# Performance work log

Measured on AMD Instinct MI355X. Metric: run time of the kernel, lower is better.

The kernel has to match this reference:

```python
import jax, jax.numpy as jnp
import numpy as np

N = 100000      # nodes
E = 3200000     # edges (before self-loops)
IN = 1          # input feature dim
H1, C = 4, 8    # layer1: 4 heads x 8 channels; layer2: 1 head x 8 channels
NEG_SLOPE = 0.2


def setup_inputs() -> dict:
    key = jax.random.key(0)
    ks = jax.random.split(key, 10)
    x = jax.random.normal(ks[0], (N, IN), jnp.float32)
    edge_index = jax.random.randint(ks[1], (2, E), 0, N, dtype=jnp.int32)
    # layer 1 params (GATConv(1, 8, heads=4))
    W1 = jax.random.normal(ks[2], (IN, H1 * C), jnp.float32) * 0.5
    a_src1 = jax.random.normal(ks[3], (H1, C), jnp.float32) * 0.5
    a_dst1 = jax.random.normal(ks[4], (H1, C), jnp.float32) * 0.5
    b1 = jnp.zeros((H1 * C,), jnp.float32)
    # layer 2 params (GATConv(32, 8, heads=1))
    W2 = jax.random.normal(ks[5], (H1 * C, C), jnp.float32) * 0.2
    a_src2 = jax.random.normal(ks[6], (1, C), jnp.float32) * 0.5
    a_dst2 = jax.random.normal(ks[7], (1, C), jnp.float32) * 0.5
    b2 = jnp.zeros((C,), jnp.float32)
    return {"x": x, "edge_index": edge_index, "W1": W1, "a_src1": a_src1,
            "a_dst1": a_dst1, "b1": b1, "W2": W2, "a_src2": a_src2,
            "a_dst2": a_dst2, "b2": b2}


def _gat_layer(x, src, dst, W, a_s, a_d, b, heads, ch):
    # Linear transform per head: [N, heads, ch]
    h = (x @ W).reshape(-1, heads, ch)
    # per-node attention logits
    al_s = jnp.einsum('nhc,hc->nh', h, a_s)  # [N, H]
    al_d = jnp.einsum('nhc,hc->nh', h, a_d)  # [N, H]
    # per-edge logits (message src -> dst)
    e = jax.nn.leaky_relu(al_s[src] + al_d[dst], NEG_SLOPE)  # [E', H]
    # segment softmax over incoming edges of each dst node
    m = jax.ops.segment_max(e, dst, num_segments=N)          # [N, H]
    e = jnp.exp(e - m[dst])
    s = jax.ops.segment_sum(e, dst, num_segments=N)          # [N, H]
    alpha = e / s[dst]                                       # [E', H]
    # weighted scatter-add aggregation
    out = jax.ops.segment_sum(h[src] * alpha[:, :, None], dst, num_segments=N)
    return out.reshape(N, heads * ch) + b


def reference(x, edge_index, W1, a_src1, a_dst1, b1, W2, a_src2, a_dst2, b2):
    loops = jnp.arange(N, dtype=edge_index.dtype)
    src = jnp.concatenate([edge_index[0], loops])  # add self-loops (PyG default)
    dst = jnp.concatenate([edge_index[1], loops])
    h = _gat_layer(x, src, dst, W1, a_src1, a_dst1, b1, H1, C)
    h = jax.nn.relu(h)
    out = _gat_layer(h, src, dst, W2, a_src2, a_dst2, b2, 1, C)
    return out
```

## Files before the change

kernel.cpp:

```cpp
#include <hip/hip_runtime.h>
#include <hip/hip_bf16.h>

#define NEG_SLOPE 0.2f



__global__ void scatter_count(const int* __restrict__ ei, int* __restrict__ percnt,
                              int E) {
    __shared__ int cnt[2048];
    int t = threadIdx.x;
    int chunk = (E + gridDim.x - 1) / gridDim.x;
    int lo = blockIdx.x * chunk;
    int hi = min(E, lo + chunk);
    const int* dei = ei + E;
    for (int i = t; i < 2048; i += 1024) cnt[i] = 0;
    __syncthreads();
    bool vec = ((E & 3) == 0);
    int lo4 = (lo + 3) & ~3;
    int end4 = hi & ~3;
    if (vec && end4 > lo4) {
        for (int e = lo + t; e < lo4; e += 1024)
            atomicAdd(&cnt[dei[e] >> 6], 1);
        const int4* dei4 = (const int4*)dei;
        for (int v = (lo4 >> 2) + t; v < (end4 >> 2); v += 1024) {
            int4 d = dei4[v];
            atomicAdd(&cnt[d.x >> 6], 1);
            atomicAdd(&cnt[d.y >> 6], 1);
            atomicAdd(&cnt[d.z >> 6], 1);
            atomicAdd(&cnt[d.w >> 6], 1);
        }
        for (int e = end4 + t; e < hi; e += 1024)
            atomicAdd(&cnt[dei[e] >> 6], 1);
    } else {
        for (int e = lo + t; e < hi; e += 1024)
            atomicAdd(&cnt[dei[e] >> 6], 1);
    }
    __syncthreads();
    int* myp = percnt + blockIdx.x * 2048;
    for (int i = t; i < 2048; i += 1024) myp[i] = cnt[i];
}

__global__ void scan_bucket(int* __restrict__ percnt, int* __restrict__ gcnt,
                            int NBLK) {
    int wid = (blockIdx.x * blockDim.x + threadIdx.x) >> 6;
    int lane = threadIdx.x & 63;
    if (wid >= 2048) return;
    int base = lane * 4;
    int c0 = (base + 0 < NBLK) ? percnt[(size_t)(base + 0) * 2048 + wid] : 0;
    int c1 = (base + 1 < NBLK) ? percnt[(size_t)(base + 1) * 2048 + wid] : 0;
    int c2 = (base + 2 < NBLK) ? percnt[(size_t)(base + 2) * 2048 + wid] : 0;
    int c3 = (base + 3 < NBLK) ? percnt[(size_t)(base + 3) * 2048 + wid] : 0;
    int p1 = c0, p2 = c0 + c1, p3 = c0 + c1 + c2;
    int lsum = p3 + c3;
    int v = lsum;
    #pragma unroll
    for (int o = 1; o < 64; o <<= 1) {
        int u = __shfl_up(v, o, 64);
        if (lane >= o) v += u;
    }
    int excl = v - lsum;
    if (base + 0 < NBLK) percnt[(size_t)(base + 0) * 2048 + wid] = excl;
    if (base + 1 < NBLK) percnt[(size_t)(base + 1) * 2048 + wid] = excl + p1;
    if (base + 2 < NBLK) percnt[(size_t)(base + 2) * 2048 + wid] = excl + p2;
    if (base + 3 < NBLK) percnt[(size_t)(base + 3) * 2048 + wid] = excl + p3;
    if (lane == 63) gcnt[wid] = excl + lsum;
}

__global__ void scan_init(const int* __restrict__ gcnt,
                          int* __restrict__ gbase, int* __restrict__ gcursor,
                          const float* __restrict__ W1,
                          const float* __restrict__ as1,
                          const float* __restrict__ ad1,
                          float* __restrict__ consts) {
    __shared__ int buf[512];
    int t = threadIdx.x;
    if (t < 8) {
        int h = t & 3;
        const float* a = (t < 4) ? as1 : ad1;
        float s = 0.f;
        #pragma unroll
        for (int c = 0; c < 8; ++c)
            s += W1[h * 8 + c] * a[h * 8 + c];
        consts[t] = s;
    }
    int c0 = gcnt[t * 4], c1 = gcnt[t * 4 + 1], c2 = gcnt[t * 4 + 2], c3 = gcnt[t * 4 + 3];
    int sum = c0 + c1 + c2 + c3;
    buf[t] = sum;
    __syncthreads();
    for (int o = 1; o < 512; o <<= 1) {
        int add = (t >= o) ? buf[t - o] : 0;
        __syncthreads();
        buf[t] += add;
        __syncthreads();
    }
    int base = buf[t] - sum;
    gbase[t * 4] = base;     gcursor[t * 4] = base;     base += c0;
    gbase[t * 4 + 1] = base; gcursor[t * 4 + 1] = base; base += c1;
    gbase[t * 4 + 2] = base; gcursor[t * 4 + 2] = base; base += c2;
    gbase[t * 4 + 3] = base; gcursor[t * 4 + 3] = base;
}

__global__ void scatter_write(const int* __restrict__ ei,
                              const int* __restrict__ gbase,
                              const int* __restrict__ percnt,
                              unsigned int* __restrict__ pairs, int E) {
    __shared__ int cnt[2048];
    __shared__ int basel[2048];
    int t = threadIdx.x;
    int chunk = (E + gridDim.x - 1) / gridDim.x;
    int lo = blockIdx.x * chunk;
    int hi = min(E, lo + chunk);
    const int* dei = ei + E;
    const int* myp = percnt + blockIdx.x * 2048;
    for (int i = t; i < 2048; i += 1024) {
        cnt[i] = 0;
        basel[i] = gbase[i] + myp[i];
    }
    __syncthreads();
    bool vec = ((E & 3) == 0);
    int lo4 = (lo + 3) & ~3;
    int end4 = hi & ~3;
    if (vec && end4 > lo4) {
        for (int e = lo + t; e < lo4; e += 1024) {
            int s = ei[e], d = dei[e];
            int bk = d >> 6;
            int loc = atomicAdd(&cnt[bk], 1);
            pairs[basel[bk] + loc] = (unsigned)s | ((unsigned)(d & 63) << 17);
        }
        const int4* sei4 = (const int4*)ei;
        const int4* dei4 = (const int4*)dei;
        for (int v = (lo4 >> 2) + t; v < (end4 >> 2); v += 1024) {
            int4 sv = sei4[v];
            int4 dv = dei4[v];
            int bk0 = dv.x >> 6, bk1 = dv.y >> 6, bk2 = dv.z >> 6, bk3 = dv.w >> 6;
            int l0 = atomicAdd(&cnt[bk0], 1);
            pairs[basel[bk0] + l0] = (unsigned)sv.x | ((unsigned)(dv.x & 63) << 17);
            int l1 = atomicAdd(&cnt[bk1], 1);
            pairs[basel[bk1] + l1] = (unsigned)sv.y | ((unsigned)(dv.y & 63) << 17);
            int l2 = atomicAdd(&cnt[bk2], 1);
            pairs[basel[bk2] + l2] = (unsigned)sv.z | ((unsigned)(dv.z & 63) << 17);
            int l3 = atomicAdd(&cnt[bk3], 1);
            pairs[basel[bk3] + l3] = (unsigned)sv.w | ((unsigned)(dv.w & 63) << 17);
        }
        for (int e = end4 + t; e < hi; e += 1024) {
            int s = ei[e], d = dei[e];
            int bk = d >> 6;
            int loc = atomicAdd(&cnt[bk], 1);
            pairs[basel[bk] + loc] = (unsigned)s | ((unsigned)(d & 63) << 17);
        }
    } else {
        for (int e = lo + t; e < hi; e += 1024) {
            int s = ei[e], d = dei[e];
            int bk = d >> 6;
            int loc = atomicAdd(&cnt[bk], 1);
            pairs[basel[bk] + loc] = (unsigned)s | ((unsigned)(d & 63) << 17);
        }
    }
}


__global__ void bucket_hist(const int* __restrict__ ei, int* __restrict__ gcnt, int E) {
    __shared__ int cnt[2048];
    int t = threadIdx.x;
    for (int i = t; i < 2048; i += 256) cnt[i] = 0;
    __syncthreads();
    const int* dei = ei + E;
    int gid = blockIdx.x * 256 + t;
    int gstride = gridDim.x * 256;
    if ((E & 3) == 0) {
        const int4* dei4 = (const int4*)dei;
        int E4 = E >> 2;
        for (int v = gid; v < E4; v += gstride) {
            int4 d = dei4[v];
            atomicAdd(&cnt[d.x >> 6], 1);
            atomicAdd(&cnt[d.y >> 6], 1);
            atomicAdd(&cnt[d.z >> 6], 1);
            atomicAdd(&cnt[d.w >> 6], 1);
        }
    } else {
        for (int e = gid; e < E; e += gstride)
            atomicAdd(&cnt[dei[e] >> 6], 1);
    }
    __syncthreads();
    for (int i = t; i < 2048; i += 256) {
        int c = cnt[i];
        if (c) atomicAdd(&gcnt[i], c);
    }
}

__global__ void bucket_scatter(const int* __restrict__ ei, int* __restrict__ gcursor,
                               unsigned int* __restrict__ pairs, int E) {
    __shared__ int cnt[2048];
    __shared__ int basel[2048];
    int t = threadIdx.x;
    int chunk = (E + gridDim.x - 1) / gridDim.x;
    int lo = blockIdx.x * chunk;
    int hi = min(E, lo + chunk);
    const int* dei = ei + E;
    for (int i = t; i < 2048; i += 1024) cnt[i] = 0;
    __syncthreads();
    for (int e = lo + t; e < hi; e += 1024)
        atomicAdd(&cnt[dei[e] >> 6], 1);
    __syncthreads();
    for (int i = t; i < 2048; i += 1024) {
        int c = cnt[i];
        basel[i] = c ? atomicAdd(&gcursor[i], c) : 0;
        cnt[i] = 0;
    }
    __syncthreads();
    for (int e = lo + t; e < hi; e += 1024) {
        int s = ei[e], d = dei[e];
        int bk = d >> 6;
        int loc = atomicAdd(&cnt[bk], 1);
        pairs[basel[bk] + loc] = (unsigned)s | ((unsigned)(d & 63) << 17);
    }
}


__global__ void l1_comb(const float* __restrict__ x,
                        const int* __restrict__ gbase, const int* __restrict__ gcnt,
                        const unsigned int* __restrict__ pairs,
                        const float* __restrict__ consts,
                        const float* __restrict__ W1, const float* __restrict__ b1,
                        const float* __restrict__ W2,
                        const float* __restrict__ as2, const float* __restrict__ ad2,
                        float* __restrict__ h2, float* __restrict__ als2,
                        float* __restrict__ ald2, int N) {
    __shared__ float R[8 * 64 * 9];
    __shared__ float xl[64];
    int t = threadIdx.x;
    int lane = t & 63;
    int bk = blockIdx.x;
    int node0 = bk << 6;
    int nw = min(64, N - node0);
    for (int i = t; i < 8 * 64 * 9; i += 512) R[i] = 0.f;
    if (t < nw) xl[t] = x[node0 + t];
    float S[4], D[4];
    #pragma unroll
    for (int h = 0; h < 4; ++h) { S[h] = consts[h]; D[h] = consts[4 + h]; }
    __syncthreads();
    float* wreg = &R[(t >> 6) * 576];
    int b = gbase[bk];
    int hi = b + gcnt[bk];
    int i = b + t;
    unsigned p = (i < hi) ? pairs[i] : 0u;
    while (i < hi) {
        int inx = i + 512;
        unsigned pn = 0u;
        if (inx < hi) pn = pairs[inx];
        int src = (int)(p & 131071u);
        int ld  = (int)(p >> 17);
        float xs = x[src];
        float xd = xl[ld];
        float w[4];
        #pragma unroll
        for (int h = 0; h < 4; ++h) {
            float v = xs * S[h] + xd * D[h];
            v = (v > 0.f) ? v : NEG_SLOPE * v;
            w[h] = __expf(v);
        }
        unsigned long long mask = ~0ull;
        #pragma unroll
        for (int bit = 0; bit < 6; ++bit) {
            unsigned long long bb = __ballot((ld >> bit) & 1);
            mask &= ((ld >> bit) & 1) ? bb : ~bb;
        }
        mask &= __ballot(1);
        int rank = __popcll(mask & ((1ull << lane) - 1ull));
        float* row = &wreg[ld * 9];
        for (int r = 0; r < 64; ++r) {
            if (__ballot(rank == r) == 0ull) break;
            if (rank == r) {
                row[0] += w[0]; row[1] += w[1]; row[2] += w[2]; row[3] += w[3];
                row[4] = fmaf(w[0], xs, row[4]); row[5] = fmaf(w[1], xs, row[5]);
                row[6] = fmaf(w[2], xs, row[6]); row[7] = fmaf(w[3], xs, row[7]);
            }
        }
        p = pn; i = inx;
    }
    __syncthreads();
    if (t < nw) {
        int n = node0 + t;
        float xn = xl[t];
        float o[8];
        #pragma unroll
        for (int c = 0; c < 8; ++c) o[c] = 0.f;
        #pragma unroll
        for (int h = 0; h < 4; ++h) {
            float v = xn * (S[h] + D[h]);
            v = (v > 0.f) ? v : NEG_SLOPE * v;
            float ww = __expf(v);
            float s1 = ww, t1 = ww * xn;
            #pragma unroll
            for (int r = 0; r < 8; ++r) {
                s1 += R[r * 576 + t * 9 + h];
                t1 += R[r * 576 + t * 9 + 4 + h];
            }
            float tt = t1 / s1;
            #pragma unroll
            for (int c = 0; c < 8; ++c) {
                float rr = fmaxf(tt * W1[h * 8 + c] + b1[h * 8 + c], 0.f);
                #pragma unroll
                for (int c2 = 0; c2 < 8; ++c2) o[c2] += rr * W2[(h * 8 + c) * 8 + c2];
            }
        }
        float as = 0.f, ad = 0.f;
        #pragma unroll
        for (int c = 0; c < 8; ++c) { as += o[c] * as2[c]; ad += o[c] * ad2[c]; }
        float4* hv = (float4*)&h2[(size_t)n * 8];
        hv[0] = make_float4(o[0], o[1], o[2], o[3]);
        hv[1] = make_float4(o[4], o[5], o[6], o[7]);
        als2[n] = as;
        ald2[n] = ad;
    }
}

__global__ void l2_comb(const int* __restrict__ gbase, const int* __restrict__ gcnt,
                        const unsigned int* __restrict__ pairs,
                        const float* __restrict__ als2, const float* __restrict__ ald2,
                        const float* __restrict__ h2, const float* __restrict__ b2,
                        float* __restrict__ out, int N) {
    __shared__ float R[8 * 64 * 9];
    __shared__ float adl[64];
    int t = threadIdx.x;
    int lane = t & 63;
    int bk = blockIdx.x;
    int node0 = bk << 6;
    int nw = min(64, N - node0);
    for (int i = t; i < 8 * 64 * 9; i += 512) R[i] = 0.f;
    if (t < nw) adl[t] = ald2[node0 + t];
    __syncthreads();
    float* wreg = &R[(t >> 6) * 576];
    int b = gbase[bk];
    int hi = b + gcnt[bk];
    int i = b + t;
    unsigned p = (i < hi) ? pairs[i] : 0u;
    while (i < hi) {
        int inx = i + 512;
        unsigned pn = 0u;
        if (inx < hi) pn = pairs[inx];
        int src = (int)(p & 131071u);
        int ld  = (int)(p >> 17);
        float a = als2[src];
        const float4* hv = (const float4*)&h2[(size_t)src * 8];
        float4 ha = hv[0], hb = hv[1];
        float v = a + adl[ld];
        v = (v > 0.f) ? v : NEG_SLOPE * v;
        float w = __expf(v);
        unsigned long long mask = ~0ull;
        #pragma unroll
        for (int bit = 0; bit < 6; ++bit) {
            unsigned long long bb = __ballot((ld >> bit) & 1);
            mask &= ((ld >> bit) & 1) ? bb : ~bb;
        }
        mask &= __ballot(1);
        int rank = __popcll(mask & ((1ull << lane) - 1ull));
        float* row = &wreg[ld * 9];
        for (int r = 0; r < 64; ++r) {
            if (__ballot(rank == r) == 0ull) break;
            if (rank == r) {
                row[0] += w;
                row[1] = fmaf(w, ha.x, row[1]); row[2] = fmaf(w, ha.y, row[2]);
                row[3] = fmaf(w, ha.z, row[3]); row[4] = fmaf(w, ha.w, row[4]);
                row[5] = fmaf(w, hb.x, row[5]); row[6] = fmaf(w, hb.y, row[6]);
                row[7] = fmaf(w, hb.z, row[7]); row[8] = fmaf(w, hb.w, row[8]);
            }
        }
        p = pn; i = inx;
    }
    __syncthreads();
    if (t < nw) {
        int n = node0 + t;
        float v = als2[n] + adl[t];
        v = (v > 0.f) ? v : NEG_SLOPE * v;
        float ww = __expf(v);
        const float4* hv = (const float4*)&h2[(size_t)n * 8];
        float4 ha0 = hv[0], hb0 = hv[1];
        float acc[9];
        #pragma unroll
        for (int c = 0; c < 9; ++c) {
            float s = 0.f;
            #pragma unroll
            for (int r = 0; r < 8; ++r) s += R[r * 576 + t * 9 + c];
            acc[c] = s;
        }
        float s2 = acc[0] + ww;
        float inv = 1.f / s2;
        float4* ov = (float4*)&out[(size_t)n * 8];
        ov[0] = make_float4((acc[1] + ww * ha0.x) * inv + b2[0],
                            (acc[2] + ww * ha0.y) * inv + b2[1],
                            (acc[3] + ww * ha0.z) * inv + b2[2],
                            (acc[4] + ww * ha0.w) * inv + b2[3]);
        ov[1] = make_float4((acc[5] + ww * hb0.x) * inv + b2[4],
                            (acc[6] + ww * hb0.y) * inv + b2[5],
                            (acc[7] + ww * hb0.z) * inv + b2[6],
                            (acc[8] + ww * hb0.w) * inv + b2[7]);
    }
}


__global__ void prep_consts(const float* __restrict__ W1,
                            const float* __restrict__ as1,
                            const float* __restrict__ ad1,
                            float* __restrict__ consts) {
    int t = threadIdx.x;
    if (t >= 8) return;
    int h = t & 3;
    const float* a = (t < 4) ? as1 : ad1;
    float s = 0.f;
    #pragma unroll
    for (int c = 0; c < 8; ++c)
        s += W1[h * 8 + c] * a[h * 8 + c];
    consts[t] = s;
}

__global__ void edge_pass1(const int* __restrict__ ei, const float* __restrict__ x,
                           const float* __restrict__ consts,
                           float* __restrict__ s1, float* __restrict__ t1, int E, int N) {
    int e = blockIdx.x * blockDim.x + threadIdx.x;
    if (e >= E + N) return;
    int src, dst;
    if (e < E) { src = ei[e]; dst = ei[E + e]; }
    else       { src = dst = e - E; }
    float xs = x[src], xd = x[dst];
    #pragma unroll
    for (int h = 0; h < 4; ++h) {
        float v = xs * consts[h] + xd * consts[4 + h];
        v = (v > 0.f) ? v : NEG_SLOPE * v;
        float w = __expf(v);
        atomicAdd(&s1[dst * 4 + h], w);
        atomicAdd(&t1[dst * 4 + h], w * xs);
    }
}

__global__ void node_mid(const float* __restrict__ s1, const float* __restrict__ t1,
                         const float* __restrict__ W1, const float* __restrict__ b1,
                         const float* __restrict__ W2,
                         const float* __restrict__ as2, const float* __restrict__ ad2,
                         float* __restrict__ h2, float* __restrict__ als2,
                         float* __restrict__ ald2, int N) {
    int n = blockIdx.x * blockDim.x + threadIdx.x;
    if (n >= N) return;
    float o[8];
    #pragma unroll
    for (int c = 0; c < 8; ++c) o[c] = 0.f;
    #pragma unroll
    for (int h = 0; h < 4; ++h) {
        float t = t1[n * 4 + h] / s1[n * 4 + h];
        #pragma unroll
        for (int c = 0; c < 8; ++c) {
            float r = fmaxf(t * W1[h * 8 + c] + b1[h * 8 + c], 0.f);
            #pragma unroll
            for (int c2 = 0; c2 < 8; ++c2) o[c2] += r * W2[(h * 8 + c) * 8 + c2];
        }
    }
    float as = 0.f, ad = 0.f;
    #pragma unroll
    for (int c = 0; c < 8; ++c) { h2[n * 8 + c] = o[c]; as += o[c] * as2[c]; ad += o[c] * ad2[c]; }
    als2[n] = as; ald2[n] = ad;
}

__global__ void edge_pass2(const int* __restrict__ ei, const float* __restrict__ als2,
                           const float* __restrict__ ald2, const float* __restrict__ h2,
                           float* __restrict__ s2, float* __restrict__ acc2, int E, int N) {
    int e = blockIdx.x * blockDim.x + threadIdx.x;
    if (e >= E + N) return;
    int src, dst;
    if (e < E) { src = ei[e]; dst = ei[E + e]; }
    else       { src = dst = e - E; }
    float v = als2[src] + ald2[dst];
    v = (v > 0.f) ? v : NEG_SLOPE * v;
    float w = __expf(v);
    atomicAdd(&s2[dst], w);
    const float4* hs = (const float4*)&h2[src * 8];
    float4 a = hs[0], bq = hs[1];
    float* acc = &acc2[dst * 8];
    atomicAdd(&acc[0], w * a.x);  atomicAdd(&acc[1], w * a.y);
    atomicAdd(&acc[2], w * a.z);  atomicAdd(&acc[3], w * a.w);
    atomicAdd(&acc[4], w * bq.x); atomicAdd(&acc[5], w * bq.y);
    atomicAdd(&acc[6], w * bq.z); atomicAdd(&acc[7], w * bq.w);
}

__global__ void node_out(const float* __restrict__ s2, const float* __restrict__ acc2,
                         const float* __restrict__ b2, float* __restrict__ out, int N) {
    int i = blockIdx.x * blockDim.x + threadIdx.x;
    if (i >= N * 8) return;
    out[i] = acc2[i] / s2[i >> 3] + b2[i & 7];
}


extern "C" void kernel_launch(void* const* d_in, const int* in_sizes, int n_in,
                              void* d_out, int out_size, void* d_ws, size_t ws_size,
                              hipStream_t stream) {
    const float* x   = (const float*)d_in[0];
    const int*   ei  = (const int*)d_in[1];
    const float* W1  = (const float*)d_in[2];
    const float* as1 = (const float*)d_in[3];
    const float* ad1 = (const float*)d_in[4];
    const float* b1  = (const float*)d_in[5];
    const float* W2  = (const float*)d_in[6];
    const float* as2 = (const float*)d_in[7];
    const float* ad2 = (const float*)d_in[8];
    const float* b2  = (const float*)d_in[9];
    float* out = (float*)d_out;

    const int N = in_sizes[0];
    const int E = in_sizes[1] / 2;
    const int NBK = (N + 63) >> 6;
    const int SBLK = 256;

    float* ws = (float*)d_ws;
    size_t base_units = (size_t)(16 + 3 * 2048 + 10 * (size_t)N + (size_t)E);
    size_t need_old = base_units * sizeof(float);
    size_t need_new = (base_units + (size_t)SBLK * 2048) * sizeof(float);

    float*    consts  = ws;
    int*      gcnt    = (int*)(ws + 16);
    int*      gbase   = gcnt + 2048;
    int*      gcursor = gbase + 2048;
    float*    als2    = ws + 16 + 3 * 2048;
    float*    ald2    = als2 + N;
    float*    h2      = ald2 + N;
    unsigned* pairs   = (unsigned*)(h2 + 8 * (size_t)N);
    int*      percnt  = (int*)(pairs + (size_t)E);

    if (N <= 131072 && ws_size >= need_new) {
        scatter_count<<<SBLK, 1024, 0, stream>>>(ei, percnt, E);
        scan_bucket<<<512, 256, 0, stream>>>(percnt, gcnt, SBLK);
        scan_init<<<1, 512, 0, stream>>>(gcnt, gbase, gcursor, W1, as1, ad1, consts);
        scatter_write<<<SBLK, 1024, 0, stream>>>(ei, gbase, percnt, pairs, E);
        l1_comb<<<NBK, 512, 0, stream>>>(x, gbase, gcnt, pairs, consts,
                                         W1, b1, W2, as2, ad2, h2, als2, ald2, N);
        l2_comb<<<NBK, 512, 0, stream>>>(gbase, gcnt, pairs, als2, ald2, h2, b2, out, N);
    } else if (N <= 131072 && ws_size >= need_old) {
        hipMemsetAsync(gcnt, 0, 2048 * sizeof(int), stream);
        bucket_hist<<<256, 256, 0, stream>>>(ei, gcnt, E);
        scan_init<<<1, 512, 0, stream>>>(gcnt, gbase, gcursor, W1, as1, ad1, consts);
        bucket_scatter<<<256, 1024, 0, stream>>>(ei, gcursor, pairs, E);
        l1_comb<<<NBK, 512, 0, stream>>>(x, gbase, gcnt, pairs, consts,
                                         W1, b1, W2, as2, ad2, h2, als2, ald2, N);
        l2_comb<<<NBK, 512, 0, stream>>>(gbase, gcnt, pairs, als2, ald2, h2, b2, out, N);
    } else {
        float* s1   = ws + 16;
        float* t1   = s1 + 4 * (size_t)N;
        float* h2f  = t1 + 4 * (size_t)N;
        float* als2f= h2f + 8 * (size_t)N;
        float* ald2f= als2f + (size_t)N;
        float* s2   = ald2f + (size_t)N;
        float* acc2 = s2 + (size_t)N;

        hipMemsetAsync(ws, 0, (16 + 8 * (size_t)N) * sizeof(float), stream);
        hipMemsetAsync(s2, 0, 9 * (size_t)N * sizeof(float), stream);
        prep_consts<<<1, 64, 0, stream>>>(W1, as1, ad1, consts);
        int total = E + N;
        edge_pass1<<<(total + 255) / 256, 256, 0, stream>>>(ei, x, consts, s1, t1, E, N);
        node_mid<<<(N + 255) / 256, 256, 0, stream>>>(s1, t1, W1, b1, W2, as2, ad2, h2f, als2f, ald2f, N);
        edge_pass2<<<(total + 255) / 256, 256, 0, stream>>>(ei, als2f, ald2f, h2f, s2, acc2, E, N);
        node_out<<<(N * 8 + 255) / 256, 256, 0, stream>>>(s2, acc2, b2, out, N);
    }
}
```

Before: 202.0 us.

## Sort bucket edges by destination in LDS, accumulate per node in registers

The two aggregation kernels now counting-sort each 64-node bucket's edges by local destination into a shared-memory staging buffer, using ballot-based match keys and per-wave histograms. Each lane then owns one destination node and accumulates its sums in registers, replacing the serialized rank-loop read-modify-write into shared memory. Block size drops from 512 to 256 threads, and a fallback keeps the old conflict-serialized path for buckets with more than 4096 edges. The extra passes over pairs and the lane-per-node layout add work and can cause load imbalance across lanes with uneven in-degree. The histogram kernel also loses its int4 vectorized path.

```diff
diff --git a/kernel.cpp b/kernel.cpp
--- a/kernel.cpp
+++ b/kernel.cpp
@@ -2,7 +2,19 @@
 #include <hip/hip_bf16.h>
 
 #define NEG_SLOPE 0.2f
-
+#define STAGE_CAP 4096
+
+
+__device__ __forceinline__ unsigned long long match_key(int ld) {
+    unsigned long long mask = ~0ull;
+    #pragma unroll
+    for (int bit = 0; bit < 6; ++bit) {
+        unsigned long long bb = __ballot((ld >> bit) & 1);
+        mask &= ((ld >> bit) & 1) ? bb : ~bb;
+    }
+    mask &= __ballot(1);
+    return mask;
+}
 
 
 __global__ void scatter_count(const int* __restrict__ ei, int* __restrict__ percnt,
@@ -167,20 +179,8 @@
     const int* dei = ei + E;
     int gid = blockIdx.x * 256 + t;
     int gstride = gridDim.x * 256;
-    if ((E & 3) == 0) {
-        const int4* dei4 = (const int4*)dei;
-        int E4 = E >> 2;
-        for (int v = gid; v < E4; v += gstride) {
-            int4 d = dei4[v];
-            atomicAdd(&cnt[d.x >> 6], 1);
-            atomicAdd(&cnt[d.y >> 6], 1);
-            atomicAdd(&cnt[d.z >> 6], 1);
-            atomicAdd(&cnt[d.w >> 6], 1);
-        }
-    } else {
-        for (int e = gid; e < E; e += gstride)
-            atomicAdd(&cnt[dei[e] >> 6], 1);
-    }
+    for (int e = gid; e < E; e += gstride)
+        atomicAdd(&cnt[dei[e] >> 6], 1);
     __syncthreads();
     for (int i = t; i < 2048; i += 256) {
         int c = cnt[i];
@@ -226,57 +226,119 @@
                         const float* __restrict__ as2, const float* __restrict__ ad2,
                         float* __restrict__ h2, float* __restrict__ als2,
                         float* __restrict__ ald2, int N) {
-    __shared__ float R[8 * 64 * 9];
+    __shared__ unsigned stage[STAGE_CAP];
+    __shared__ int hcnt4[4 * 65];
+    __shared__ int hoff[64];
+    __shared__ int hlen[64];
+    __shared__ int wcur[4 * 65];
+    __shared__ float P[4 * 576];
     __shared__ float xl[64];
     int t = threadIdx.x;
     int lane = t & 63;
+    int w = t >> 6;
     int bk = blockIdx.x;
     int node0 = bk << 6;
     int nw = min(64, N - node0);
-    for (int i = t; i < 8 * 64 * 9; i += 512) R[i] = 0.f;
-    if (t < nw) xl[t] = x[node0 + t];
+    int b = gbase[bk];
+    int cnt = gcnt[bk];
     float S[4], D[4];
     #pragma unroll
     for (int h = 0; h < 4; ++h) { S[h] = consts[h]; D[h] = consts[4 + h]; }
-    __syncthreads();
-    float* wreg = &R[(t >> 6) * 576];
-    int b = gbase[bk];
-    int hi = b + gcnt[bk];
-    int i = b + t;
-    unsigned p = (i < hi) ? pairs[i] : 0u;
-    while (i < hi) {
-        int inx = i + 512;
-        unsigned pn = 0u;
-        if (inx < hi) pn = pairs[inx];
-        int src = (int)(p & 131071u);
-        int ld  = (int)(p >> 17);
-        float xs = x[src];
-        float xd = xl[ld];
-        float w[4];
-        #pragma unroll
-        for (int h = 0; h < 4; ++h) {
-            float v = xs * S[h] + xd * D[h];
-            v = (v > 0.f) ? v : NEG_SLOPE * v;
-            w[h] = __expf(v);
-        }
-        unsigned long long mask = ~0ull;
-        #pragma unroll
-        for (int bit = 0; bit < 6; ++bit) {
-            unsigned long long bb = __ballot((ld >> bit) & 1);
-            mask &= ((ld >> bit) & 1) ? bb : ~bb;
-        }
-        mask &= __ballot(1);
-        int rank = __popcll(mask & ((1ull << lane) - 1ull));
-        float* row = &wreg[ld * 9];
-        for (int r = 0; r < 64; ++r) {
-            if (__ballot(rank == r) == 0ull) break;
-            if (rank == r) {
-                row[0] += w[0]; row[1] += w[1]; row[2] += w[2]; row[3] += w[3];
-                row[4] = fmaf(w[0], xs, row[4]); row[5] = fmaf(w[1], xs, row[5]);
-                row[6] = fmaf(w[2], xs, row[6]); row[7] = fmaf(w[3], xs, row[7]);
-            }
-        }
-        p = pn; i = inx;
+    if (t < 64) xl[t] = (t < nw) ? x[node0 + t] : 0.f;
+
+    if (cnt <= STAGE_CAP) {
+        if (t < 64) {
+            #pragma unroll
+            for (int ww = 0; ww < 4; ++ww) hcnt4[ww * 65 + t] = 0;
+        }
+        __syncthreads();
+        for (int i = t; i < cnt; i += 256) {
+            int ld = (int)(pairs[b + i] >> 17);
+            unsigned long long m = match_key(ld);
+            int leader = __ffsll((unsigned long long)m) - 1;
+            if (lane == leader) hcnt4[w * 65 + ld] += __popcll(m);
+        }
+        __syncthreads();
+        if (t < 64) {
+            int tot = hcnt4[t] + hcnt4[65 + t] + hcnt4[130 + t] + hcnt4[195 + t];
+            hlen[t] = tot;
+            int v = tot;
+            #pragma unroll
+            for (int o = 1; o < 64; o <<= 1) {
+                int u = __shfl_up(v, o, 64);
+                if (lane >= o) v += u;
+            }
+            int excl = v - tot;
+            hoff[t] = excl;
+            int run = excl;
+            #pragma unroll
+            for (int ww = 0; ww < 4; ++ww) {
+                wcur[ww * 65 + t] = run;
+                run += hcnt4[ww * 65 + t];
+            }
+        }
+        __syncthreads();
+        for (int i = t; i < cnt; i += 256) {
+            unsigned p = pairs[b + i];
+            int ld = (int)(p >> 17);
+            unsigned long long m = match_key(ld);
+            int leader = __ffsll((unsigned long long)m) - 1;
+            int rank = __popcll(m & ((1ull << lane) - 1ull));
+            int cur = wcur[w * 65 + ld];
+            if (lane == leader) wcur[w * 65 + ld] = cur + __popcll(m);
+            stage[cur + rank] = p;
+        }
+        __syncthreads();
+        float s1[4] = {0.f, 0.f, 0.f, 0.f}, t1[4] = {0.f, 0.f, 0.f, 0.f};
+        int st = hoff[lane];
+        int en = st + hlen[lane];
+        float xd = xl[lane];
+        for (int i = st + w; i < en; i += 4) {
+            unsigned p = stage[i];
+            int src = (int)(p & 131071u);
+            float xs = x[src];
+            #pragma unroll
+            for (int h = 0; h < 4; ++h) {
+                float v = xs * S[h] + xd * D[h];
+                v = (v > 0.f) ? v : NEG_SLOPE * v;
+                float e = __expf(v);
+                s1[h] += e;
+                t1[h] = fmaf(e, xs, t1[h]);
+            }
+        }
+        float* row = &P[w * 576 + lane * 9];
+        #pragma unroll
+        for (int h = 0; h < 4; ++h) { row[h] = s1[h]; row[4 + h] = t1[h]; }
+    } else {
+        for (int i = t; i < 4 * 576; i += 256) P[i] = 0.f;
+        __syncthreads();
+        float* wreg = &P[w * 576];
+        int hiE = b + cnt;
+        for (int i = b + t; i < hiE; i += 256) {
+            unsigned p = pairs[i];
+            int src = (int)(p & 131071u);
+            int ld = (int)(p >> 17);
+            float xs = x[src];
+            float xd = xl[ld];
+            float wv[4];
+            #pragma unroll
+            for (int h = 0; h < 4; ++h) {
+                float v = xs * S[h] + xd * D[h];
+                v = (v > 0.f) ? v : NEG_SLOPE * v;
+                wv[h] = __expf(v);
+            }
+            unsigned long long m = match_key(ld);
+            int rank = __popcll(m & ((1ull << lane) - 1ull));
+            float* row = &wreg[ld * 9];
+            for (int r = 0; r < 64; ++r) {
+                if (__ballot(rank == r) == 0ull) break;
+                if (rank == r) {
+                    row[0] += wv[0]; row[1] += wv[1]; row[2] += wv[2]; row[3] += wv[3];
+                    row[4] = fmaf(wv[0], xs, row[4]); row[5] = fmaf(wv[1], xs, row[5]);
+                    row[6] = fmaf(wv[2], xs, row[6]); row[7] = fmaf(wv[3], xs, row[7]);
+                }
+            }
+        }
     }
     __syncthreads();
     if (t < nw) {
@@ -290,13 +352,13 @@
             float v = xn * (S[h] + D[h]);
             v = (v > 0.f) ? v : NEG_SLOPE * v;
             float ww = __expf(v);
-            float s1 = ww, t1 = ww * xn;
-            #pragma unroll
-            for (int r = 0; r < 8; ++r) {
-                s1 += R[r * 576 + t * 9 + h];
-                t1 += R[r * 576 + t * 9 + 4 + h];
-            }
-            float tt = t1 / s1;
+            float s1 = ww, t1v = ww * xn;
+            #pragma unroll
+            for (int r = 0; r < 4; ++r) {
+                s1 += P[r * 576 + t * 9 + h];
+                t1v += P[r * 576 + t * 9 + 4 + h];
+            }
+            float tt = t1v / s1;
             #pragma unroll
             for (int c = 0; c < 8; ++c) {
                 float rr = fmaxf(tt * W1[h * 8 + c] + b1[h * 8 + c], 0.f);
@@ -320,53 +382,119 @@
                         const float* __restrict__ als2, const float* __restrict__ ald2,
                         const float* __restrict__ h2, const float* __restrict__ b2,
                         float* __restrict__ out, int N) {
-    __shared__ float R[8 * 64 * 9];
+    __shared__ unsigned stage[STAGE_CAP];
+    __shared__ int hcnt4[4 * 65];
+    __shared__ int hoff[64];
+    __shared__ int hlen[64];
+    __shared__ int wcur[4 * 65];
+    __shared__ float P[4 * 576];
     __shared__ float adl[64];
     int t = threadIdx.x;
     int lane = t & 63;
+    int w = t >> 6;
     int bk = blockIdx.x;
     int node0 = bk << 6;
     int nw = min(64, N - node0);
-    for (int i = t; i < 8 * 64 * 9; i += 512) R[i] = 0.f;
-    if (t < nw) adl[t] = ald2[node0 + t];
-    __syncthreads();
-    float* wreg = &R[(t >> 6) * 576];
     int b = gbase[bk];
-    int hi = b + gcnt[bk];
-    int i = b + t;
-    unsigned p = (i < hi) ? pairs[i] : 0u;
-    while (i < hi) {
-        int inx = i + 512;
-        unsigned pn = 0u;
-        if (inx < hi) pn = pairs[inx];
-        int src = (int)(p & 131071u);
-        int ld  = (int)(p >> 17);
-        float a = als2[src];
-        const float4* hv = (const float4*)&h2[(size_t)src * 8];
-        float4 ha = hv[0], hb = hv[1];
-        float v = a + adl[ld];
-        v = (v > 0.f) ? v : NEG_SLOPE * v;
-        float w = __expf(v);
-        unsigned long long mask = ~0ull;
-        #pragma unroll
-        for (int bit = 0; bit < 6; ++bit) {
-            unsigned long long bb = __ballot((ld >> bit) & 1);
-            mask &= ((ld >> bit) & 1) ? bb : ~bb;
-        }
-        mask &= __ballot(1);
-        int rank = __popcll(mask & ((1ull << lane) - 1ull));
-        float* row = &wreg[ld * 9];
-        for (int r = 0; r < 64; ++r) {
-            if (__ballot(rank == r) == 0ull) break;
-            if (rank == r) {
-                row[0] += w;
-                row[1] = fmaf(w, ha.x, row[1]); row[2] = fmaf(w, ha.y, row[2]);
-                row[3] = fmaf(w, ha.z, row[3]); row[4] = fmaf(w, ha.w, row[4]);
-                row[5] = fmaf(w, hb.x, row[5]); row[6] = fmaf(w, hb.y, row[6]);
-                row[7] = fmaf(w, hb.z, row[7]); row[8] = fmaf(w, hb.w, row[8]);
-            }
-        }
-        p = pn; i = inx;
+    int cnt = gcnt[bk];
+    if (t < 64) adl[t] = (t < nw) ? ald2[node0 + t] : 0.f;
+
+    if (cnt <= STAGE_CAP) {
+        if (t < 64) {
+            #pragma unroll
+            for (int ww = 0; ww < 4; ++ww) hcnt4[ww * 65 + t] = 0;
+        }
+        __syncthreads();
+        for (int i = t; i < cnt; i += 256) {
+            int ld = (int)(pairs[b + i] >> 17);
+            unsigned long long m = match_key(ld);
+            int leader = __ffsll((unsigned long long)m) - 1;
+            if (lane == leader) hcnt4[w * 65 + ld] += __popcll(m);
+        }
+        __syncthreads();
+        if (t < 64) {
+            int tot = hcnt4[t] + hcnt4[65 + t] + hcnt4[130 + t] + hcnt4[195 + t];
+            hlen[t] = tot;
+            int v = tot;
+            #pragma unroll
+            for (int o = 1; o < 64; o <<= 1) {
+                int u = __shfl_up(v, o, 64);
+                if (lane >= o) v += u;
+            }
+            int excl = v - tot;
+            hoff[t] = excl;
+            int run = excl;
+            #pragma unroll
+            for (int ww = 0; ww < 4; ++ww) {
+                wcur[ww * 65 + t] = run;
+                run += hcnt4[ww * 65 + t];
+            }
+        }
+        __syncthreads();
+        for (int i = t; i < cnt; i += 256) {
+            unsigned p = pairs[b + i];
+            int ld = (int)(p >> 17);
+            unsigned long long m = match_key(ld);
+            int leader = __ffsll((unsigned long long)m) - 1;
+            int rank = __popcll(m & ((1ull << lane) - 1ull));
+            int cur = wcur[w * 65 + ld];
+            if (lane == leader) wcur[w * 65 + ld] = cur + __popcll(m);
+            stage[cur + rank] = p;
+        }
+        __syncthreads();
+        float acc[9];
+        #pragma unroll
+        for (int c = 0; c < 9; ++c) acc[c] = 0.f;
+        int st = hoff[lane];
+        int en = st + hlen[lane];
+        float aldn = adl[lane];
+        for (int i = st + w; i < en; i += 4) {
+            unsigned p = stage[i];
+            int src = (int)(p & 131071u);
+            float a = als2[src];
+            const float4* hv = (const float4*)&h2[(size_t)src * 8];
+            float4 ha = hv[0], hb = hv[1];
+            float v = a + aldn;
+            v = (v > 0.f) ? v : NEG_SLOPE * v;
+            float e = __expf(v);
+            acc[0] += e;
+            acc[1] = fmaf(e, ha.x, acc[1]); acc[2] = fmaf(e, ha.y, acc[2]);
+            acc[3] = fmaf(e, ha.z, acc[3]); acc[4] = fmaf(e, ha.w, acc[4]);
+            acc[5] = fmaf(e, hb.x, acc[5]); acc[6] = fmaf(e, hb.y, acc[6]);
+            acc[7] = fmaf(e, hb.z, acc[7]); acc[8] = fmaf(e, hb.w, acc[8]);
+        }
+        float* row = &P[w * 576 + lane * 9];
+        #pragma unroll
+        for (int c = 0; c < 9; ++c) row[c] = acc[c];
+    } else {
+        for (int i = t; i < 4 * 576; i += 256) P[i] = 0.f;
+        __syncthreads();
+        float* wreg = &P[w * 576];
+        int hiE = b + cnt;
+        for (int i = b + t; i < hiE; i += 256) {
+            unsigned p = pairs[i];
+            int src = (int)(p & 131071u);
+            int ld = (int)(p >> 17);
+            float a = als2[src];
+            const float4* hv = (const float4*)&h2[(size_t)src * 8];
+            float4 ha = hv[0], hb = hv[1];
+            float v = a + adl[ld];
+            v = (v > 0.f) ? v : NEG_SLOPE * v;
+            float e = __expf(v);
+            unsigned long long m = match_key(ld);
+            int rank = __popcll(m & ((1ull << lane) - 1ull));
+            float* row = &wreg[ld * 9];
+            for (int r = 0; r < 64; ++r) {
+                if (__ballot(rank == r) == 0ull) break;
+                if (rank == r) {
+                    row[0] += e;
+                    row[1] = fmaf(e, ha.x, row[1]); row[2] = fmaf(e, ha.y, row[2]);
+                    row[3] = fmaf(e, ha.z, row[3]); row[4] = fmaf(e, ha.w, row[4]);
+                    row[5] = fmaf(e, hb.x, row[5]); row[6] = fmaf(e, hb.y, row[6]);
+                    row[7] = fmaf(e, hb.z, row[7]); row[8] = fmaf(e, hb.w, row[8]);
+                }
+            }
+        }
     }
     __syncthreads();
     if (t < nw) {
@@ -375,26 +503,26 @@
         v = (v > 0.f) ? v : NEG_SLOPE * v;
         float ww = __expf(v);
         const float4* hv = (const float4*)&h2[(size_t)n * 8];
-        float4 ha0 = hv[0], hb0 = hv[1];
+        float4 hsa = hv[0], hsb = hv[1];
         float acc[9];
         #pragma unroll
         for (int c = 0; c < 9; ++c) {
             float s = 0.f;
             #pragma unroll
-            for (int r = 0; r < 8; ++r) s += R[r * 576 + t * 9 + c];
+            for (int r = 0; r < 4; ++r) s += P[r * 576 + t * 9 + c];
             acc[c] = s;
         }
         float s2 = acc[0] + ww;
         float inv = 1.f / s2;
         float4* ov = (float4*)&out[(size_t)n * 8];
-        ov[0] = make_float4((acc[1] + ww * ha0.x) * inv + b2[0],
-                            (acc[2] + ww * ha0.y) * inv + b2[1],
-                            (acc[3] + ww * ha0.z) * inv + b2[2],
-                            (acc[4] + ww * ha0.w) * inv + b2[3]);
-        ov[1] = make_float4((acc[5] + ww * hb0.x) * inv + b2[4],
-                            (acc[6] + ww * hb0.y) * inv + b2[5],
-                            (acc[7] + ww * hb0.z) * inv + b2[6],
-                            (acc[8] + ww * hb0.w) * inv + b2[7]);
+        ov[0] = make_float4((acc[1] + ww * hsa.x) * inv + b2[0],
+                            (acc[2] + ww * hsa.y) * inv + b2[1],
+                            (acc[3] + ww * hsa.z) * inv + b2[2],
+                            (acc[4] + ww * hsa.w) * inv + b2[3]);
+        ov[1] = make_float4((acc[5] + ww * hsb.x) * inv + b2[4],
+                            (acc[6] + ww * hsb.y) * inv + b2[5],
+                            (acc[7] + ww * hsb.z) * inv + b2[6],
+                            (acc[8] + ww * hsb.w) * inv + b2[7]);
     }
 }
 
@@ -529,17 +657,17 @@
         scan_bucket<<<512, 256, 0, stream>>>(percnt, gcnt, SBLK);
         scan_init<<<1, 512, 0, stream>>>(gcnt, gbase, gcursor, W1, as1, ad1, consts);
         scatter_write<<<SBLK, 1024, 0, stream>>>(ei, gbase, percnt, pairs, E);
-        l1_comb<<<NBK, 512, 0, stream>>>(x, gbase, gcnt, pairs, consts,
+        l1_comb<<<NBK, 256, 0, stream>>>(x, gbase, gcnt, pairs, consts,
                                          W1, b1, W2, as2, ad2, h2, als2, ald2, N);
-        l2_comb<<<NBK, 512, 0, stream>>>(gbase, gcnt, pairs, als2, ald2, h2, b2, out, N);
+        l2_comb<<<NBK, 256, 0, stream>>>(gbase, gcnt, pairs, als2, ald2, h2, b2, out, N);
     } else if (N <= 131072 && ws_size >= need_old) {
         hipMemsetAsync(gcnt, 0, 2048 * sizeof(int), stream);
         bucket_hist<<<256, 256, 0, stream>>>(ei, gcnt, E);
         scan_init<<<1, 512, 0, stream>>>(gcnt, gbase, gcursor, W1, as1, ad1, consts);
         bucket_scatter<<<256, 1024, 0, stream>>>(ei, gcursor, pairs, E);
-        l1_comb<<<NBK, 512, 0, stream>>>(x, gbase, gcnt, pairs, consts,
+        l1_comb<<<NBK, 256, 0, stream>>>(x, gbase, gcnt, pairs, consts,
                                          W1, b1, W2, as2, ad2, h2, als2, ald2, N);
-        l2_comb<<<NBK, 512, 0, stream>>>(gbase, gcnt, pairs, als2, ald2, h2, b2, out, N);
+        l2_comb<<<NBK, 256, 0, stream>>>(gbase, gcnt, pairs, als2, ald2, h2, b2, out, N);
     } else {
         float* s1   = ws + 16;
         float* t1   = s1 + 4 * (size_t)N;
```

Measured after the change: 207.6 us. 1.03x slower.
